# Performance work log

Hardware: AMD Instinct MI355X
Metric: run time of the kernel (lower is better)

Reference implementation:

```python
import jax, jax.numpy as jnp
import numpy as np

B, T, C = 2, 2048, 1024
H = 16
DK = C // H


def setup_inputs() -> dict:
    key = jax.random.key(0)
    ks = jax.random.split(key, 5)
    x = jax.random.normal(ks[0], (B, T, C), dtype=jnp.float32)
    # causal mask, broadcastable to [B, H, T, T]; mask==0 -> -inf
    mask = jnp.tril(jnp.ones((T, T), dtype=jnp.int32))[None, None]
    s = 1.0 / np.sqrt(C)
    qkv_w = jax.random.normal(ks[1], (3 * C, C), dtype=jnp.float32) * s  # torch Linear layout [out,in]
    qkv_b = jnp.zeros((3 * C,), dtype=jnp.float32)
    out_w = jax.random.normal(ks[2], (C, C), dtype=jnp.float32) * s
    out_b = jnp.zeros((C,), dtype=jnp.float32)
    return {"x": x, "mask": mask, "qkv_w": qkv_w, "qkv_b": qkv_b,
            "out_w": out_w, "out_b": out_b}


def reference(x, mask, qkv_w, qkv_b, out_w, out_b):
    b, t, c = x.shape
    qkv = x @ qkv_w.T + qkv_b                       # [B,T,3C]
    qkv = qkv.reshape(b, t, 3, H, DK)
    q, k, v = qkv[:, :, 0], qkv[:, :, 1], qkv[:, :, 2]   # [B,T,H,DK]
    scores = jnp.einsum('bqhd,bkhd->bhqk', q, k) / np.sqrt(DK)
    scores = jnp.where(mask == 0, -jnp.inf, scores)
    attn_weights = jax.nn.softmax(scores, axis=-1)       # [B,H,T,T]
    attn_out = jnp.einsum('bhqk,bkhd->bqhd', attn_weights, v).reshape(b, t, c)
    out = attn_out @ out_w.T + out_b
    return out, attn_weights
```

## Files before the change

kernel.cpp:

```cpp
#include <hip/hip_runtime.h>
#include <hip/hip_bf16.h>

typedef short short8  __attribute__((ext_vector_type(8)));
typedef short short4v __attribute__((ext_vector_type(4)));
typedef __bf16 bf16x8 __attribute__((ext_vector_type(8)));
typedef float f32x4   __attribute__((ext_vector_type(4)));

__device__ __forceinline__ void mfma16(f32x4& d, short8 a, short8 b) {
    d = __builtin_amdgcn_mfma_f32_16x16x32_bf16(
            __builtin_bit_cast(bf16x8, a), __builtin_bit_cast(bf16x8, b), d, 0, 0, 0);
}

__device__ __forceinline__ unsigned short f2bf(float f) {
    union { float f; unsigned u; } a; a.f = f;
    unsigned u = a.u;
    return (unsigned short)((u + 0x7fffu + ((u >> 16) & 1u)) >> 16);
}
__device__ __forceinline__ float bf2f(unsigned short us) {
    union { unsigned u; float f; } a; a.u = ((unsigned)us) << 16;
    return a.f;
}

__global__ void cvt_all(const float* __restrict__ x, const float* __restrict__ w1,
                        const float* __restrict__ w2,
                        unsigned short* __restrict__ ox, unsigned short* __restrict__ o1,
                        unsigned short* __restrict__ o2) {
    int i = blockIdx.x * 256 + threadIdx.x;
    const float* src; unsigned short* dst; int j;
    if (i < 1048576)      { src = x;  dst = ox; j = i; }
    else if (i < 1835008) { src = w1; dst = o1; j = i - 1048576; }
    else                  { src = w2; dst = o2; j = i - 1835008; }
    float4 v = ((const float4*)src)[j];
    ushort4 o;
    o.x = f2bf(v.x); o.y = f2bf(v.y); o.z = f2bf(v.z); o.w = f2bf(v.w);
    ((ushort4*)dst)[j] = o;
}

template<int OUTBF, int VTF>
__global__ __launch_bounds__(256)
void gemm_bt(const unsigned short* __restrict__ A, const unsigned short* __restrict__ Bw,
             const float* __restrict__ bias, void* __restrict__ Cout,
             unsigned short* __restrict__ vt, int M, int N, int K)
{
    __shared__ unsigned short As[128 * 64];
    __shared__ unsigned short Bs[128 * 64];

    const int tid  = threadIdx.x;
    const int lane = tid & 63;
    const int wid  = tid >> 6;
    const int row0 = blockIdx.y << 7;
    const int col0 = blockIdx.x << 7;
    const int wr = (wid >> 1) << 6;
    const int wc = (wid & 1) << 6;
    const int rl = lane & 15;
    const int g  = lane >> 4;

    f32x4 acc[4][4] = {};

    for (int k0 = 0; k0 < K; k0 += 64) {
        __syncthreads();
#pragma unroll
        for (int rd = 0; rd < 4; ++rd) {
            int s  = rd * 256 + tid;
            int r  = s >> 3, cs = s & 7;
            int cg = cs ^ (r & 7);
            __builtin_amdgcn_global_load_lds(
                (__attribute__((address_space(1))) void*)(A + (size_t)(row0 + r) * K + k0 + cg * 8),
                (__attribute__((address_space(3))) void*)(As + s * 8), 16, 0, 0);
            __builtin_amdgcn_global_load_lds(
                (__attribute__((address_space(1))) void*)(Bw + (size_t)(col0 + r) * K + k0 + cg * 8),
                (__attribute__((address_space(3))) void*)(Bs + s * 8), 16, 0, 0);
        }
        __syncthreads();

#pragma unroll
        for (int h = 0; h < 2; ++h) {
            short8 af[4], bf[4];
#pragma unroll
            for (int m = 0; m < 4; ++m) {
                int rr = wr + m * 16 + rl;
                int ch = ((h << 2) + g) ^ (rr & 7);
                af[m] = *(const short8*)(As + rr * 64 + ch * 8);
            }
#pragma unroll
            for (int n = 0; n < 4; ++n) {
                int rr = wc + n * 16 + rl;
                int ch = ((h << 2) + g) ^ (rr & 7);
                bf[n] = *(const short8*)(Bs + rr * 64 + ch * 8);
            }
#pragma unroll
            for (int m = 0; m < 4; ++m)
#pragma unroll
                for (int n = 0; n < 4; ++n)
                    mfma16(acc[m][n], af[m], bf[n]);
        }
    }

    const int b  = row0 >> 11;
    const int tg = (row0 & 2047) + wr + (g << 2);
#pragma unroll
    for (int n = 0; n < 4; ++n) {
        int col = col0 + wc + n * 16 + rl;
        float bv = bias[col];
        if (VTF && col >= 2048) {
            int hd = col - 2048;
            unsigned short* vr = vt + ((size_t)((b << 4) + (hd >> 6)) * 64 + (hd & 63)) * 2048;
#pragma unroll
            for (int m = 0; m < 4; ++m) {
                short4v p;
#pragma unroll
                for (int r = 0; r < 4; ++r) p[r] = (short)f2bf(acc[m][n][r] + bv);
                *(short4v*)(vr + tg + m * 16) = p;
            }
        } else {
#pragma unroll
            for (int m = 0; m < 4; ++m) {
#pragma unroll
                for (int r = 0; r < 4; ++r) {
                    int row = row0 + wr + m * 16 + (g << 2) + r;
                    float v = acc[m][n][r] + bv;
                    if (OUTBF) ((unsigned short*)Cout)[(size_t)row * N + col] = f2bf(v);
                    else       __builtin_nontemporal_store(v, (float*)Cout + (size_t)row * N + col);
                }
            }
        }
    }
}

__device__ __forceinline__ int S_addr(int row, int col) {
    return (row << 11) + ((((col >> 3) ^ (row & 7))) << 3) + (col & 7);
}

__global__ __launch_bounds__(256, 2)
void attn_kernel(const unsigned short* __restrict__ qkv,
                 const unsigned short* __restrict__ vt,
                 float* __restrict__ wout,
                 unsigned short* __restrict__ aout)
{
    __shared__ unsigned short Ss[16 * 2048];
    __shared__ float part[4][16];

    const int bid = blockIdx.x;
    const int qt = bid & 127;
    const int bh = bid >> 7;
    const int b = bh >> 4, h = bh & 15;
    const int q0 = qt << 4;
    const int tid = threadIdx.x;
    const int wid = tid >> 6;
    const int lane = tid & 63;
    const int rl = lane & 15;
    const int g  = lane >> 4;

    int nt = (qt + 4) & ~3;
    if (nt > 128) nt = 128;
    const int ntiles = nt;
    const int KPAD = ntiles << 4;

    const unsigned short* Qb = qkv + (size_t)((b << 11) + q0) * 3072 + (h << 6);
    short8 qf0 = *(const short8*)(Qb + (size_t)rl * 3072 + g * 8);
    short8 qf1 = *(const short8*)(Qb + (size_t)rl * 3072 + 32 + g * 8);

    const unsigned short* Kb = qkv + (size_t)(b << 11) * 3072 + 1024 + (h << 6);

    float psum[4] = {0.f, 0.f, 0.f, 0.f};

#pragma unroll 2
    for (int kt = wid; kt < ntiles; kt += 4) {
        f32x4 acc = {};
        const unsigned short* kp = Kb + (size_t)(kt * 16 + rl) * 3072;
        short8 kf0 = *(const short8*)(kp + g * 8);
        short8 kf1 = *(const short8*)(kp + 32 + g * 8);
        mfma16(acc, qf0, kf0);
        mfma16(acc, qf1, kf1);
        int col = kt * 16 + rl;
#pragma unroll
        for (int r = 0; r < 4; ++r) {
            int qrow = g * 4 + r;
            float e = (col <= q0 + qrow) ? __expf(acc[r] * 0.125f) : 0.0f;
            Ss[S_addr(qrow, col)] = f2bf(e);
            psum[r] += e;
        }
    }
#pragma unroll
    for (int m = 8; m; m >>= 1)
#pragma unroll
        for (int r = 0; r < 4; ++r) psum[r] += __shfl_xor(psum[r], m);
    if (rl == 0) {
#pragma unroll
        for (int r = 0; r < 4; ++r) part[wid][g * 4 + r] = psum[r];
    }
    __syncthreads();

    f32x4 p0 = {}, p1 = {};
    const unsigned short* vrow = vt + ((size_t)(bh << 6) + wid * 16 + rl) * 2048;
    const int nkc = KPAD >> 5;
    for (int kc = 0; kc < nkc; kc += 2) {
        int c0 = (kc << 2) + g;
        short8 a0 = *(const short8*)(Ss + (rl << 11) + ((c0 ^ (rl & 7)) << 3));
        short8 b0 = *(const short8*)(vrow + (kc << 5) + (g << 3));
        mfma16(p0, a0, b0);
        int c1 = c0 + 4;
        short8 a1 = *(const short8*)(Ss + (rl << 11) + ((c1 ^ (rl & 7)) << 3));
        short8 b1 = *(const short8*)(vrow + ((kc + 1) << 5) + (g << 3));
        mfma16(p1, a1, b1);
    }
    f32x4 pacc = p0 + p1;
#pragma unroll
    for (int r = 0; r < 4; ++r) {
        int qrow = g * 4 + r;
        float inv = 1.0f / (part[0][qrow] + part[1][qrow] + part[2][qrow] + part[3][qrow]);
        float v = pacc[r] * inv;
        aout[(size_t)((b << 11) + q0 + qrow) * 1024 + (h << 6) + wid * 16 + rl] = f2bf(v);
    }

    for (int r = wid; r < 16; r += 4) {
        float inv = 1.0f / (part[0][r] + part[1][r] + part[2][r] + part[3][r]);
        float* orow = wout + ((size_t)bh * 2048 + q0 + r) * 2048;
        for (int j8 = lane * 8; j8 < KPAD; j8 += 512) {
            short8 ev = *(const short8*)(Ss + S_addr(r, j8));
            f32x4 o0, o1;
            o0[0] = bf2f((unsigned short)ev[0]) * inv;
            o0[1] = bf2f((unsigned short)ev[1]) * inv;
            o0[2] = bf2f((unsigned short)ev[2]) * inv;
            o0[3] = bf2f((unsigned short)ev[3]) * inv;
            o1[0] = bf2f((unsigned short)ev[4]) * inv;
            o1[1] = bf2f((unsigned short)ev[5]) * inv;
            o1[2] = bf2f((unsigned short)ev[6]) * inv;
            o1[3] = bf2f((unsigned short)ev[7]) * inv;
            __builtin_nontemporal_store(o0, (f32x4*)(orow + j8));
            __builtin_nontemporal_store(o1, (f32x4*)(orow + j8 + 4));
        }
        f32x4 z = {0.f, 0.f, 0.f, 0.f};
        for (int j = KPAD + (lane << 2); j < 2048; j += 256)
            __builtin_nontemporal_store(z, (f32x4*)(orow + j));
    }
}

extern "C" void kernel_launch(void* const* d_in, const int* in_sizes, int n_in,
                              void* d_out, int out_size, void* d_ws, size_t ws_size,
                              hipStream_t stream)
{
    const float* x     = (const float*)d_in[0];
    const float* qkv_w = (const float*)d_in[2];
    const float* qkv_b = (const float*)d_in[3];
    const float* out_w = (const float*)d_in[4];
    const float* out_b = (const float*)d_in[5];

    char* ws = (char*)d_ws;
    unsigned short* xbf   = (unsigned short*)(ws);
    unsigned short* wqkv  = (unsigned short*)(ws + 8388608);
    unsigned short* woutw = (unsigned short*)(ws + 14680064);
    unsigned short* qkv   = (unsigned short*)(ws + 16777216);
    unsigned short* vt    = (unsigned short*)(ws + 41943040);
    unsigned short* aout  = (unsigned short*)(ws + 50331648);

    float* out  = (float*)d_out;
    float* wout = (float*)d_out + 4194304;

    cvt_all<<<8192, 256, 0, stream>>>(x, qkv_w, out_w, xbf, wqkv, woutw);

    gemm_bt<1, 1><<<dim3(24, 32), 256, 0, stream>>>(xbf, wqkv, qkv_b, qkv, vt, 4096, 3072, 1024);
    attn_kernel<<<4096, 256, 0, stream>>>(qkv, vt, wout, aout);
    gemm_bt<0, 0><<<dim3(8, 32), 256, 0, stream>>>(aout, woutw, out_b, out, nullptr, 4096, 1024, 1024);
}
```

Before: 254.9 us.

## Remap blocks across XCDs, prefetch K tiles, reorder weight store before PV

Both GEMMs now launch as a 1D grid and remap block indices so that consecutive blocks landing on the same XCD (blockIdx.x mod 8) share row and column tiles, and the attention kernel remaps its block index the same way. The QK loop software-prefetches the next K fragment, and MFMA sections are wrapped in s_setprio to raise wave priority. The large fp32 attention-weight store now runs before the PV matmul, so the stores can overlap with the vt loads and MFMAs. The remapping assumes that dispatch is round-robin across 8 XCDs and that grid sizes divide evenly by 8.

```diff
diff --git a/kernel.cpp b/kernel.cpp
--- a/kernel.cpp
+++ b/kernel.cpp
@@ -48,8 +48,10 @@
     const int tid  = threadIdx.x;
     const int lane = tid & 63;
     const int wid  = tid >> 6;
-    const int row0 = blockIdx.y << 7;
-    const int col0 = blockIdx.x << 7;
+    const int swz  = (int)((blockIdx.x & 7) * (gridDim.x >> 3) + (blockIdx.x >> 3));
+    const int nby  = M >> 7;
+    const int row0 = (swz % nby) << 7;
+    const int col0 = (swz / nby) << 7;
     const int wr = (wid >> 1) << 6;
     const int wc = (wid & 1) << 6;
     const int rl = lane & 15;
@@ -140,7 +142,7 @@
     __shared__ unsigned short Ss[16 * 2048];
     __shared__ float part[4][16];
 
-    const int bid = blockIdx.x;
+    const int bid = (int)(((blockIdx.x & 7) << 9) + (blockIdx.x >> 3));
     const int qt = bid & 127;
     const int bh = bid >> 7;
     const int b = bh >> 4, h = bh & 15;
@@ -164,21 +166,32 @@
 
     float psum[4] = {0.f, 0.f, 0.f, 0.f};
 
-#pragma unroll 2
-    for (int kt = wid; kt < ntiles; kt += 4) {
-        f32x4 acc = {};
+    {
+        int kt = wid;
         const unsigned short* kp = Kb + (size_t)(kt * 16 + rl) * 3072;
-        short8 kf0 = *(const short8*)(kp + g * 8);
-        short8 kf1 = *(const short8*)(kp + 32 + g * 8);
-        mfma16(acc, qf0, kf0);
-        mfma16(acc, qf1, kf1);
-        int col = kt * 16 + rl;
-#pragma unroll
-        for (int r = 0; r < 4; ++r) {
-            int qrow = g * 4 + r;
-            float e = (col <= q0 + qrow) ? __expf(acc[r] * 0.125f) : 0.0f;
-            Ss[S_addr(qrow, col)] = f2bf(e);
-            psum[r] += e;
+        short8 ka0 = *(const short8*)(kp + g * 8);
+        short8 ka1 = *(const short8*)(kp + 32 + g * 8);
+        for (; kt < ntiles; kt += 4) {
+            short8 kb0 = ka0, kb1 = ka1;
+            if (kt + 4 < ntiles) {
+                const unsigned short* kp2 = Kb + (size_t)((kt + 4) * 16 + rl) * 3072;
+                kb0 = *(const short8*)(kp2 + g * 8);
+                kb1 = *(const short8*)(kp2 + 32 + g * 8);
+            }
+            f32x4 acc = {};
+            __builtin_amdgcn_s_setprio(1);
+            mfma16(acc, qf0, ka0);
+            mfma16(acc, qf1, ka1);
+            __builtin_amdgcn_s_setprio(0);
+            int col = kt * 16 + rl;
+#pragma unroll
+            for (int r = 0; r < 4; ++r) {
+                int qrow = g * 4 + r;
+                float e = (col <= q0 + qrow) ? __expf(acc[r] * 0.125f) : 0.0f;
+                Ss[S_addr(qrow, col)] = f2bf(e);
+                psum[r] += e;
+            }
+            ka0 = kb0; ka1 = kb1;
         }
     }
 #pragma unroll
@@ -190,28 +203,6 @@
         for (int r = 0; r < 4; ++r) part[wid][g * 4 + r] = psum[r];
     }
     __syncthreads();
-
-    f32x4 p0 = {}, p1 = {};
-    const unsigned short* vrow = vt + ((size_t)(bh << 6) + wid * 16 + rl) * 2048;
-    const int nkc = KPAD >> 5;
-    for (int kc = 0; kc < nkc; kc += 2) {
-        int c0 = (kc << 2) + g;
-        short8 a0 = *(const short8*)(Ss + (rl << 11) + ((c0 ^ (rl & 7)) << 3));
-        short8 b0 = *(const short8*)(vrow + (kc << 5) + (g << 3));
-        mfma16(p0, a0, b0);
-        int c1 = c0 + 4;
-        short8 a1 = *(const short8*)(Ss + (rl << 11) + ((c1 ^ (rl & 7)) << 3));
-        short8 b1 = *(const short8*)(vrow + ((kc + 1) << 5) + (g << 3));
-        mfma16(p1, a1, b1);
-    }
-    f32x4 pacc = p0 + p1;
-#pragma unroll
-    for (int r = 0; r < 4; ++r) {
-        int qrow = g * 4 + r;
-        float inv = 1.0f / (part[0][qrow] + part[1][qrow] + part[2][qrow] + part[3][qrow]);
-        float v = pacc[r] * inv;
-        aout[(size_t)((b << 11) + q0 + qrow) * 1024 + (h << 6) + wid * 16 + rl] = f2bf(v);
-    }
 
     for (int r = wid; r < 16; r += 4) {
         float inv = 1.0f / (part[0][r] + part[1][r] + part[2][r] + part[3][r]);
@@ -234,6 +225,30 @@
         for (int j = KPAD + (lane << 2); j < 2048; j += 256)
             __builtin_nontemporal_store(z, (f32x4*)(orow + j));
     }
+
+    f32x4 p0 = {}, p1 = {};
+    const unsigned short* vrow = vt + ((size_t)(bh << 6) + wid * 16 + rl) * 2048;
+    const int nkc = KPAD >> 5;
+    for (int kc = 0; kc < nkc; kc += 2) {
+        int c0 = (kc << 2) + g;
+        short8 a0 = *(const short8*)(Ss + (rl << 11) + ((c0 ^ (rl & 7)) << 3));
+        short8 b0 = *(const short8*)(vrow + (kc << 5) + (g << 3));
+        int c1 = c0 + 4;
+        short8 a1 = *(const short8*)(Ss + (rl << 11) + ((c1 ^ (rl & 7)) << 3));
+        short8 b1 = *(const short8*)(vrow + ((kc + 1) << 5) + (g << 3));
+        __builtin_amdgcn_s_setprio(1);
+        mfma16(p0, a0, b0);
+        mfma16(p1, a1, b1);
+        __builtin_amdgcn_s_setprio(0);
+    }
+    f32x4 pacc = p0 + p1;
+#pragma unroll
+    for (int r = 0; r < 4; ++r) {
+        int qrow = g * 4 + r;
+        float inv = 1.0f / (part[0][qrow] + part[1][qrow] + part[2][qrow] + part[3][qrow]);
+        float v = pacc[r] * inv;
+        aout[(size_t)((b << 11) + q0 + qrow) * 1024 + (h << 6) + wid * 16 + rl] = f2bf(v);
+    }
 }
 
 extern "C" void kernel_launch(void* const* d_in, const int* in_sizes, int n_in,
@@ -259,7 +274,7 @@
 
     cvt_all<<<8192, 256, 0, stream>>>(x, qkv_w, out_w, xbf, wqkv, woutw);
 
-    gemm_bt<1, 1><<<dim3(24, 32), 256, 0, stream>>>(xbf, wqkv, qkv_b, qkv, vt, 4096, 3072, 1024);
+    gemm_bt<1, 1><<<768, 256, 0, stream>>>(xbf, wqkv, qkv_b, qkv, vt, 4096, 3072, 1024);
     attn_kernel<<<4096, 256, 0, stream>>>(qkv, vt, wout, aout);
-    gemm_bt<0, 0><<<dim3(8, 32), 256, 0, stream>>>(aout, woutw, out_b, out, nullptr, 4096, 1024, 1024);
-}
+    gemm_bt<0, 0><<<256, 256, 0, stream>>>(aout, woutw, out_b, out, nullptr, 4096, 1024, 1024);
+}
```

New measurement: 234.0 us. -8.2%, faster.
